# Optimization experiments

Measured on AMD Instinct MI355X. Metric: run time of the kernel, lower is better.

The kernel has to match this reference:

```python
import jax, jax.numpy as jnp
import numpy as np

N = 50000
E = 800000
NFEAT, NHID, NCLASS = 128, 128, 40


def setup_inputs() -> dict:
    key = jax.random.key(0)
    ks = jax.random.split(key, 8)
    x = jax.random.normal(ks[0], (N, NFEAT), dtype=jnp.float32)
    edge_index = jax.random.randint(ks[1], (2, E), 0, N, dtype=jnp.int64)
    def glorot(k, fan_in, fan_out):
        s = jnp.sqrt(6.0 / (fan_in + fan_out)).astype(jnp.float32)
        return jax.random.uniform(k, (fan_in, fan_out), jnp.float32, -s, s)
    W1 = glorot(ks[2], NFEAT, NHID); b1 = jnp.zeros((NHID,), jnp.float32)
    W2 = glorot(ks[3], NHID, NHID);  b2 = jnp.zeros((NHID,), jnp.float32)
    W3 = glorot(ks[4], NHID, NCLASS); b3 = jnp.zeros((NCLASS,), jnp.float32)
    return {"x": x, "edge_index": edge_index,
            "W1": W1, "b1": b1, "W2": W2, "b2": b2, "W3": W3, "b3": b3}


def _gcn_norm(edge_index, num_nodes, dtype):
    # Add self-loops, then symmetric normalization D^-1/2 (A+I) D^-1/2 (PyG gcn_norm).
    loop = jnp.arange(num_nodes, dtype=edge_index.dtype)
    src = jnp.concatenate([edge_index[0], loop])
    dst = jnp.concatenate([edge_index[1], loop])
    deg = jax.ops.segment_sum(jnp.ones_like(src, dtype=dtype), dst, num_segments=num_nodes)
    dinv = jnp.where(deg > 0, deg ** -0.5, 0.0).astype(dtype)
    norm = dinv[src] * dinv[dst]  # [E+N]
    return src, dst, norm


def _gcn_conv(h, src, dst, norm, W, b, num_nodes):
    h = h @ W                              # dense transform first (out_dim small)
    msg = h[src] * norm[:, None]           # gather + per-edge scale
    out = jax.ops.segment_sum(msg, dst, num_segments=num_nodes)  # scatter-add
    return out + b


def reference(x, edge_index, W1, b1, W2, b2, W3, b3):
    src, dst, norm = _gcn_norm(edge_index, N, x.dtype)
    h = jax.nn.relu(_gcn_conv(x, src, dst, norm, W1, b1, N))  # dropout: eval mode (identity)
    h = jax.nn.relu(_gcn_conv(h, src, dst, norm, W2, b2, N))
    h = _gcn_conv(h, src, dst, norm, W3, b3, N)
    return jax.nn.log_softmax(h, axis=-1)
```

## Files before the change

kernel.cpp:

```cpp
#include <hip/hip_runtime.h>
#include <stdint.h>

#define NN 50000
#define NE 800000
#define GG 782
#define NB 196
#define EB 3125

typedef __attribute__((ext_vector_type(8))) short bfx8;
typedef __attribute__((ext_vector_type(4))) float f32x4;

__device__ inline unsigned short f2bf(float f) {
    union { float f; uint32_t u; } x; x.f = f;
    uint32_t u = x.u;
    return (unsigned short)((u + 0x7fffu + ((u >> 16) & 1u)) >> 16);
}
__device__ inline uint32_t pack2bf(float lo, float hi) {
    return (uint32_t)f2bf(lo) | ((uint32_t)f2bf(hi) << 16);
}
__device__ inline float bf2f(unsigned short h) {
    union { uint32_t u; float f; } c; c.u = ((uint32_t)h) << 16;
    return c.f;
}
__device__ inline float2 bfp2f2(uint32_t v) {
    union { uint32_t u; float f; } a, b;
    a.u = (v & 0xffffu) << 16;
    b.u = v & 0xffff0000u;
    return make_float2(a.f, b.f);
}
__device__ inline bfx8 ld8(const unsigned short* p) {
    union { uint4 u; bfx8 v; } c;
    c.u = *(const uint4*)p;
    return c.v;
}
__device__ inline bfx8 cvt8(float4 u, float4 v) {
    union { unsigned short s[8]; bfx8 r; } c;
    c.s[0] = f2bf(u.x); c.s[1] = f2bf(u.y); c.s[2] = f2bf(u.z); c.s[3] = f2bf(u.w);
    c.s[4] = f2bf(v.x); c.s[5] = f2bf(v.y); c.s[6] = f2bf(v.z); c.s[7] = f2bf(v.w);
    return c.r;
}

__global__ void prep(const float* __restrict__ W1, const float* __restrict__ W2,
                     const float* __restrict__ W3,
                     unsigned short* __restrict__ WT1, unsigned short* __restrict__ WT2,
                     unsigned short* __restrict__ WT3, int* __restrict__ hist) {
    int bid = blockIdx.x;
    if (bid < 152) {
        int w = bid * 256 + threadIdx.x;
        if (w < 16384) {
            int nn = w >> 7, k = w & 127;
            WT1[nn * 128 + k] = f2bf(W1[k * 128 + nn]);
        } else if (w < 32768) {
            int w2 = w - 16384, nn = w2 >> 7, k = w2 & 127;
            WT2[nn * 128 + k] = f2bf(W2[k * 128 + nn]);
        } else if (w < 38912) {
            int w2 = w - 32768, nn = w2 >> 7, k = w2 & 127;
            WT3[nn * 128 + k] = (nn < 40) ? f2bf(W3[k * 40 + nn]) : (unsigned short)0;
        }
    } else {
        int i = (bid - 152) * 256 + threadIdx.x;
        if (i < NN) hist[i] = 0;
    }
}

__global__ __launch_bounds__(256) void gemm1_hist(const float* __restrict__ X,
                                                  const unsigned short* __restrict__ WT,
                                                  unsigned short* __restrict__ G, int n,
                                                  const int* __restrict__ dst,
                                                  int* __restrict__ hist,
                                                  unsigned short* __restrict__ rank, int e) {
    if (blockIdx.x >= GG) {
        int i = (blockIdx.x - GG) * 256 + threadIdx.x;
        if (i < e) rank[i] = (unsigned short)atomicAdd(hist + dst[i], 1);
        return;
    }
    int wave = threadIdx.x >> 6;
    int lane = threadIdx.x & 63;
    int quad = lane >> 4;
    int c = lane & 15;
    int rowbase = blockIdx.x * 64 + wave * 16;

    int arow = rowbase + c;
    if (arow >= n) arow = n - 1;
    const float* ap = X + (size_t)arow * 128 + quad * 8;
    bfx8 a[4];
#pragma unroll
    for (int kc = 0; kc < 4; kc++) {
        float4 u = *(const float4*)(ap + kc * 32);
        float4 v = *(const float4*)(ap + kc * 32 + 4);
        a[kc] = cvt8(u, v);
    }

    f32x4 acc[8];
#pragma unroll
    for (int ct = 0; ct < 8; ct++) acc[ct] = (f32x4){0.f, 0.f, 0.f, 0.f};
#pragma unroll
    for (int ct = 0; ct < 8; ct++) {
        const unsigned short* bp = WT + (size_t)(ct * 16 + c) * 128 + quad * 8;
#pragma unroll
        for (int kc = 0; kc < 4; kc++) {
            bfx8 b = ld8(bp + kc * 32);
            acc[ct] = __builtin_amdgcn_mfma_f32_16x16x32_bf16(a[kc], b, acc[ct], 0, 0, 0);
        }
    }

    int r0 = rowbase + quad * 4;
    bool odd = lane & 1;
#pragma unroll
    for (int ct = 0; ct < 8; ct++) {
        float x0 = acc[ct][0], x1 = acc[ct][1], x2 = acc[ct][2], x3 = acc[ct][3];
        float y0 = __shfl_xor(x0, 1, 64), y1 = __shfl_xor(x1, 1, 64);
        float y2 = __shfl_xor(x2, 1, 64), y3 = __shfl_xor(x3, 1, 64);
        int colp = ct * 16 + (c & ~1);
        if (!odd) {
            if (r0 + 0 < n) *(uint32_t*)(&G[(size_t)(r0 + 0) * 128 + colp]) = pack2bf(x0, y0);
            if (r0 + 1 < n) *(uint32_t*)(&G[(size_t)(r0 + 1) * 128 + colp]) = pack2bf(x1, y1);
        } else {
            if (r0 + 2 < n) *(uint32_t*)(&G[(size_t)(r0 + 2) * 128 + colp]) = pack2bf(y2, x2);
            if (r0 + 3 < n) *(uint32_t*)(&G[(size_t)(r0 + 3) * 128 + colp]) = pack2bf(y3, x3);
        }
    }
}

__global__ void scan_dinv(const int* __restrict__ hist, int* row_ptr, int* bsum,
                          float* dinv, int n) {
    __shared__ int s[256];
    int tid = threadIdx.x;
    int i = blockIdx.x * 256 + tid;
    int v = (i < n) ? hist[i] : 0;
    s[tid] = v;
    __syncthreads();
#pragma unroll
    for (int off = 1; off < 256; off <<= 1) {
        int y = (tid >= off) ? s[tid - off] : 0;
        __syncthreads();
        s[tid] += y;
        __syncthreads();
    }
    if (i < n) {
        row_ptr[i] = s[tid] - v;
        dinv[i] = rsqrtf(1.0f + (float)v);
    }
    if (tid == 255) bsum[blockIdx.x] = s[255];
}

__global__ void bucket_k(const int* __restrict__ src, const int* __restrict__ dst,
                         const int* __restrict__ row_ptr, const int* __restrict__ bsum,
                         const unsigned short* __restrict__ rank,
                         unsigned short* __restrict__ csr_src, int* __restrict__ boff_g,
                         int e) {
    __shared__ int s[256];
    __shared__ int bex[256];
    int tid = threadIdx.x;
    int v = (tid < NB) ? bsum[tid] : 0;
    s[tid] = v;
    __syncthreads();
#pragma unroll
    for (int off = 1; off < 256; off <<= 1) {
        int y = (tid >= off) ? s[tid - off] : 0;
        __syncthreads();
        s[tid] += y;
        __syncthreads();
    }
    bex[tid] = s[tid] - v;
    __syncthreads();

    if (blockIdx.x == gridDim.x - 1) {
        if (tid < NB) boff_g[tid] = bex[tid];
        return;
    }
    int i = blockIdx.x * 256 + tid;
    if (i < e) {
        int d = dst[i];
        csr_src[row_ptr[d] + bex[d >> 8] + (int)rank[i]] = (unsigned short)src[i];
    }
}

__global__ __launch_bounds__(256) void gemm128_mfma(const unsigned short* __restrict__ A,
                                                    const unsigned short* __restrict__ WT,
                                                    const float* __restrict__ dinv,
                                                    unsigned short* __restrict__ G, int n) {
    int wave = threadIdx.x >> 6;
    int lane = threadIdx.x & 63;
    int quad = lane >> 4;
    int c = lane & 15;
    int rowbase = blockIdx.x * 64 + wave * 16;

    int arow = rowbase + c;
    if (arow >= n) arow = n - 1;
    const unsigned short* ap = A + (size_t)arow * 128 + quad * 8;
    bfx8 a[4];
#pragma unroll
    for (int kc = 0; kc < 4; kc++) a[kc] = ld8(ap + kc * 32);

    f32x4 acc[8];
#pragma unroll
    for (int ct = 0; ct < 8; ct++) acc[ct] = (f32x4){0.f, 0.f, 0.f, 0.f};
#pragma unroll
    for (int ct = 0; ct < 8; ct++) {
        const unsigned short* bp = WT + (size_t)(ct * 16 + c) * 128 + quad * 8;
#pragma unroll
        for (int kc = 0; kc < 4; kc++) {
            bfx8 b = ld8(bp + kc * 32);
            acc[ct] = __builtin_amdgcn_mfma_f32_16x16x32_bf16(a[kc], b, acc[ct], 0, 0, 0);
        }
    }

    int r0 = rowbase + quad * 4;
    float di[4];
#pragma unroll
    for (int r = 0; r < 4; r++) {
        int rr = r0 + r;
        di[r] = dinv[rr < n ? rr : 0];
    }
    bool odd = lane & 1;
#pragma unroll
    for (int ct = 0; ct < 8; ct++) {
        float x0 = acc[ct][0], x1 = acc[ct][1], x2 = acc[ct][2], x3 = acc[ct][3];
        float y0 = __shfl_xor(x0, 1, 64), y1 = __shfl_xor(x1, 1, 64);
        float y2 = __shfl_xor(x2, 1, 64), y3 = __shfl_xor(x3, 1, 64);
        int colp = ct * 16 + (c & ~1);
        if (!odd) {
            if (r0 + 0 < n) *(uint32_t*)(&G[(size_t)(r0 + 0) * 128 + colp]) = pack2bf(di[0] * x0, di[0] * y0);
            if (r0 + 1 < n) *(uint32_t*)(&G[(size_t)(r0 + 1) * 128 + colp]) = pack2bf(di[1] * x1, di[1] * y1);
        } else {
            if (r0 + 2 < n) *(uint32_t*)(&G[(size_t)(r0 + 2) * 128 + colp]) = pack2bf(di[2] * y2, di[2] * x2);
            if (r0 + 3 < n) *(uint32_t*)(&G[(size_t)(r0 + 3) * 128 + colp]) = pack2bf(di[3] * y3, di[3] * x3);
        }
    }
}

__global__ __launch_bounds__(256) void gemm40_mfma(const unsigned short* __restrict__ A,
                                                   const unsigned short* __restrict__ WT,
                                                   const float* __restrict__ dinv,
                                                   unsigned short* __restrict__ G, int n) {
    int wave = threadIdx.x >> 6;
    int lane = threadIdx.x & 63;
    int quad = lane >> 4;
    int c = lane & 15;
    int rowbase = blockIdx.x * 64 + wave * 16;

    int arow = rowbase + c;
    if (arow >= n) arow = n - 1;
    const unsigned short* ap = A + (size_t)arow * 128 + quad * 8;
    bfx8 a[4];
#pragma unroll
    for (int kc = 0; kc < 4; kc++) a[kc] = ld8(ap + kc * 32);

    f32x4 acc[3];
#pragma unroll
    for (int ct = 0; ct < 3; ct++) acc[ct] = (f32x4){0.f, 0.f, 0.f, 0.f};
#pragma unroll
    for (int ct = 0; ct < 3; ct++) {
        const unsigned short* bp = WT + (size_t)(ct * 16 + c) * 128 + quad * 8;
#pragma unroll
        for (int kc = 0; kc < 4; kc++) {
            bfx8 b = ld8(bp + kc * 32);
            acc[ct] = __builtin_amdgcn_mfma_f32_16x16x32_bf16(a[kc], b, acc[ct], 0, 0, 0);
        }
    }

    int r0 = rowbase + quad * 4;
    float di[4];
#pragma unroll
    for (int r = 0; r < 4; r++) {
        int rr = r0 + r;
        di[r] = dinv[rr < n ? rr : 0];
    }
    bool odd = lane & 1;
#pragma unroll
    for (int ct = 0; ct < 3; ct++) {
        float x0 = acc[ct][0], x1 = acc[ct][1], x2 = acc[ct][2], x3 = acc[ct][3];
        float y0 = __shfl_xor(x0, 1, 64), y1 = __shfl_xor(x1, 1, 64);
        float y2 = __shfl_xor(x2, 1, 64), y3 = __shfl_xor(x3, 1, 64);
        int colp = ct * 16 + (c & ~1);
        if (colp >= 40) continue;
        if (!odd) {
            if (r0 + 0 < n) *(uint32_t*)(&G[(size_t)(r0 + 0) * 40 + colp]) = pack2bf(di[0] * x0, di[0] * y0);
            if (r0 + 1 < n) *(uint32_t*)(&G[(size_t)(r0 + 1) * 40 + colp]) = pack2bf(di[1] * x1, di[1] * y1);
        } else {
            if (r0 + 2 < n) *(uint32_t*)(&G[(size_t)(r0 + 2) * 40 + colp]) = pack2bf(di[2] * y2, di[2] * x2);
            if (r0 + 3 < n) *(uint32_t*)(&G[(size_t)(r0 + 3) * 40 + colp]) = pack2bf(di[3] * y3, di[3] * x3);
        }
    }
}

__global__ __launch_bounds__(256) void agg128_l1(const unsigned short* __restrict__ G,
                                                 const int* __restrict__ row_ptr,
                                                 const int* __restrict__ boff,
                                                 const int* __restrict__ hist,
                                                 const unsigned short* __restrict__ csr_src,
                                                 const float* __restrict__ dinv,
                                                 const float* __restrict__ b,
                                                 unsigned short* __restrict__ Y, int n) {
    int node = blockIdx.x * 4 + (threadIdx.x >> 6);
    if (node >= n) return;
    int l = threadIdx.x & 63;
    const uint32_t* Gr = (const uint32_t*)G;

    float dn = dinv[node];
    float2 sf = bfp2f2(Gr[(size_t)node * 64 + l]);
    float2 acc = make_float2(dn * sf.x, dn * sf.y);
    int p = row_ptr[node] + boff[node >> 8];
    int p1 = p + hist[node];
    for (; p + 7 < p1; p += 8) {
        int s0 = csr_src[p],     s1 = csr_src[p + 1], s2 = csr_src[p + 2], s3 = csr_src[p + 3];
        int s4 = csr_src[p + 4], s5 = csr_src[p + 5], s6 = csr_src[p + 6], s7 = csr_src[p + 7];
        float d0 = dinv[s0], d1 = dinv[s1], d2 = dinv[s2], d3 = dinv[s3];
        float d4 = dinv[s4], d5 = dinv[s5], d6 = dinv[s6], d7 = dinv[s7];
        float2 f0 = bfp2f2(Gr[(size_t)s0 * 64 + l]), f1 = bfp2f2(Gr[(size_t)s1 * 64 + l]);
        float2 f2 = bfp2f2(Gr[(size_t)s2 * 64 + l]), f3 = bfp2f2(Gr[(size_t)s3 * 64 + l]);
        float2 f4 = bfp2f2(Gr[(size_t)s4 * 64 + l]), f5 = bfp2f2(Gr[(size_t)s5 * 64 + l]);
        float2 f6 = bfp2f2(Gr[(size_t)s6 * 64 + l]), f7 = bfp2f2(Gr[(size_t)s7 * 64 + l]);
        acc.x += (fmaf(d0, f0.x, d1 * f1.x) + fmaf(d2, f2.x, d3 * f3.x)) +
                 (fmaf(d4, f4.x, d5 * f5.x) + fmaf(d6, f6.x, d7 * f7.x));
        acc.y += (fmaf(d0, f0.y, d1 * f1.y) + fmaf(d2, f2.y, d3 * f3.y)) +
                 (fmaf(d4, f4.y, d5 * f5.y) + fmaf(d6, f6.y, d7 * f7.y));
    }
    for (; p < p1; ++p) {
        int s = csr_src[p];
        float ds = dinv[s];
        float2 f = bfp2f2(Gr[(size_t)s * 64 + l]);
        acc.x = fmaf(ds, f.x, acc.x);
        acc.y = fmaf(ds, f.y, acc.y);
    }
    float vx = fmaf(dn, acc.x, b[2 * l]);
    float vy = fmaf(dn, acc.y, b[2 * l + 1]);
    ((uint32_t*)Y)[(size_t)node * 64 + l] = pack2bf(vx > 0.f ? vx : 0.f, vy > 0.f ? vy : 0.f);
}

__global__ __launch_bounds__(256) void agg128(const unsigned short* __restrict__ G,
                                              const int* __restrict__ row_ptr,
                                              const int* __restrict__ boff,
                                              const int* __restrict__ hist,
                                              const unsigned short* __restrict__ csr_src,
                                              const float* __restrict__ dinv,
                                              const float* __restrict__ b,
                                              unsigned short* __restrict__ Y, int n) {
    int node = blockIdx.x * 4 + (threadIdx.x >> 6);
    if (node >= n) return;
    int l = threadIdx.x & 63;
    const uint32_t* Gr = (const uint32_t*)G;

    float2 acc = bfp2f2(Gr[(size_t)node * 64 + l]);
    int p = row_ptr[node] + boff[node >> 8];
    int p1 = p + hist[node];
    for (; p + 7 < p1; p += 8) {
        int s0 = csr_src[p],     s1 = csr_src[p + 1], s2 = csr_src[p + 2], s3 = csr_src[p + 3];
        int s4 = csr_src[p + 4], s5 = csr_src[p + 5], s6 = csr_src[p + 6], s7 = csr_src[p + 7];
        float2 f0 = bfp2f2(Gr[(size_t)s0 * 64 + l]), f1 = bfp2f2(Gr[(size_t)s1 * 64 + l]);
        float2 f2 = bfp2f2(Gr[(size_t)s2 * 64 + l]), f3 = bfp2f2(Gr[(size_t)s3 * 64 + l]);
        float2 f4 = bfp2f2(Gr[(size_t)s4 * 64 + l]), f5 = bfp2f2(Gr[(size_t)s5 * 64 + l]);
        float2 f6 = bfp2f2(Gr[(size_t)s6 * 64 + l]), f7 = bfp2f2(Gr[(size_t)s7 * 64 + l]);
        acc.x += ((f0.x + f1.x) + (f2.x + f3.x)) + ((f4.x + f5.x) + (f6.x + f7.x));
        acc.y += ((f0.y + f1.y) + (f2.y + f3.y)) + ((f4.y + f5.y) + (f6.y + f7.y));
    }
    for (; p < p1; ++p) {
        float2 f = bfp2f2(Gr[(size_t)csr_src[p] * 64 + l]);
        acc.x += f.x; acc.y += f.y;
    }
    float dn = dinv[node];
    float vx = fmaf(dn, acc.x, b[2 * l]);
    float vy = fmaf(dn, acc.y, b[2 * l + 1]);
    ((uint32_t*)Y)[(size_t)node * 64 + l] = pack2bf(vx > 0.f ? vx : 0.f, vy > 0.f ? vy : 0.f);
}

__global__ __launch_bounds__(256) void agg40_lsm(const unsigned short* __restrict__ G,
                                                 const int* __restrict__ row_ptr,
                                                 const int* __restrict__ boff,
                                                 const int* __restrict__ hist,
                                                 const unsigned short* __restrict__ csr_src,
                                                 const float* __restrict__ dinv,
                                                 const float* __restrict__ b,
                                                 float* __restrict__ Y, int n) {
    int node = blockIdx.x * 4 + (threadIdx.x >> 6);
    if (node >= n) return;
    int lane = threadIdx.x & 63;
    bool act = lane < 40;
    int lc = act ? lane : 0;

    float acc = act ? bf2f(G[(size_t)node * 40 + lane]) : 0.f;
    int p = row_ptr[node] + boff[node >> 8];
    int p1 = p + hist[node];
    for (; p + 3 < p1; p += 4) {
        int s0 = csr_src[p], s1 = csr_src[p + 1], s2 = csr_src[p + 2], s3 = csr_src[p + 3];
        float f0 = bf2f(G[(size_t)s0 * 40 + lc]);
        float f1 = bf2f(G[(size_t)s1 * 40 + lc]);
        float f2 = bf2f(G[(size_t)s2 * 40 + lc]);
        float f3 = bf2f(G[(size_t)s3 * 40 + lc]);
        acc += (f0 + f1) + (f2 + f3);
    }
    for (; p < p1; ++p) acc += bf2f(G[(size_t)csr_src[p] * 40 + lc]);

    float v = act ? fmaf(dinv[node], acc, b[lane]) : -1e30f;
    float m = v;
#pragma unroll
    for (int off = 32; off > 0; off >>= 1) m = fmaxf(m, __shfl_xor(m, off, 64));
    float ex = act ? expf(v - m) : 0.f;
    float s_ = ex;
#pragma unroll
    for (int off = 32; off > 0; off >>= 1) s_ += __shfl_xor(s_, off, 64);
    float ls = logf(s_);
    if (act) Y[(size_t)node * 40 + lane] = v - m - ls;
}


extern "C" void kernel_launch(void* const* d_in, const int* in_sizes, int n_in,
                              void* d_out, int out_size, void* d_ws, size_t ws_size,
                              hipStream_t stream) {
    const float* x  = (const float*)d_in[0];
    const int*   ei = (const int*)d_in[1];
    const float* W1 = (const float*)d_in[2];
    const float* b1 = (const float*)d_in[3];
    const float* W2 = (const float*)d_in[4];
    const float* b2 = (const float*)d_in[5];
    const float* W3 = (const float*)d_in[6];
    const float* b3 = (const float*)d_in[7];
    float* out = (float*)d_out;

    const int n = NN, e = NE;
    const int* srcI = ei;
    const int* dstI = ei + e;

    char* ws = (char*)d_ws;
    int*            hist    = (int*)ws;
    int*            row_ptr = (int*)(ws + 200704);
    int*            bsum    = (int*)(ws + 401408);
    int*            boff    = (int*)(ws + 402432);
    float*          dinv    = (float*)(ws + 403456);
    unsigned short* rank    = (unsigned short*)(ws + 604160);
    unsigned short* csr_src = (unsigned short*)(ws + 2204160);
    unsigned short* WT1     = (unsigned short*)(ws + 3804160);
    unsigned short* WT2     = (unsigned short*)(ws + 3836928);
    unsigned short* WT3     = (unsigned short*)(ws + 3869696);
    unsigned short* bufG    = (unsigned short*)(ws + 3881984);
    unsigned short* bufA    = (unsigned short*)(ws + 16681984);

    prep<<<152 + NB, 256, 0, stream>>>(W1, W2, W3, WT1, WT2, WT3, hist);
    gemm1_hist<<<GG + EB, 256, 0, stream>>>(x, WT1, bufG, n, dstI, hist, rank, e);
    scan_dinv<<<NB, 256, 0, stream>>>(hist, row_ptr, bsum, dinv, n);
    bucket_k<<<EB + 1, 256, 0, stream>>>(srcI, dstI, row_ptr, bsum, rank, csr_src, boff, e);
    agg128_l1<<<(n + 3) / 4, 256, 0, stream>>>(bufG, row_ptr, boff, hist, csr_src, dinv, b1, bufA, n);
    gemm128_mfma<<<GG, 256, 0, stream>>>(bufA, WT2, dinv, bufG, n);
    agg128<<<(n + 3) / 4, 256, 0, stream>>>(bufG, row_ptr, boff, hist, csr_src, dinv, b2, bufA, n);
    gemm40_mfma<<<GG, 256, 0, stream>>>(bufA, WT3, dinv, bufG, n);
    agg40_lsm<<<(n + 3) / 4, 256, 0, stream>>>(bufG, row_ptr, boff, hist, csr_src, dinv, b3, out, n);
}
```

Baseline: 296.9 us.

## Replicate degree histogram across 16 copies to reduce atomic contention

The in-degree histogram is split into 16 replicas, with each edge block atomically incrementing the replica chosen by its block index. The scan kernel merges the replicas into per-node degrees and per-replica offsets, and the bucket kernel adds the replica offset when placing edges into CSR. The aim is to spread atomic traffic on the same destination counters. In exchange it zeroes and reads 16 times as much histogram memory, and it stores the histogram and offsets in the bufA region that is reused later.

```diff
diff --git a/kernel.cpp b/kernel.cpp
--- a/kernel.cpp
+++ b/kernel.cpp
@@ -6,6 +6,8 @@
 #define GG 782
 #define NB 196
 #define EB 3125
+#define RR 16
+#define RZB 3125
 
 typedef __attribute__((ext_vector_type(8))) short bfx8;
 typedef __attribute__((ext_vector_type(4))) float f32x4;
@@ -59,7 +61,7 @@
         }
     } else {
         int i = (bid - 152) * 256 + threadIdx.x;
-        if (i < NN) hist[i] = 0;
+        if (i < RR * NN) hist[i] = 0;
     }
 }
 
@@ -70,8 +72,12 @@
                                                   int* __restrict__ hist,
                                                   unsigned short* __restrict__ rank, int e) {
     if (blockIdx.x >= GG) {
-        int i = (blockIdx.x - GG) * 256 + threadIdx.x;
-        if (i < e) rank[i] = (unsigned short)atomicAdd(hist + dst[i], 1);
+        int be = blockIdx.x - GG;
+        int i = be * 256 + threadIdx.x;
+        if (i < e) {
+            int r = be & (RR - 1);
+            rank[i] = (unsigned short)atomicAdd(hist + r * NN + dst[i], 1);
+        }
         return;
     }
     int wave = threadIdx.x >> 6;
@@ -123,11 +129,23 @@
 }
 
 __global__ void scan_dinv(const int* __restrict__ hist, int* row_ptr, int* bsum,
-                          float* dinv, int n) {
+                          float* dinv, int* __restrict__ deg,
+                          unsigned short* __restrict__ repoff, int n) {
     __shared__ int s[256];
     int tid = threadIdx.x;
     int i = blockIdx.x * 256 + tid;
-    int v = (i < n) ? hist[i] : 0;
+    int v = 0;
+    if (i < n) {
+        int off = 0;
+#pragma unroll
+        for (int r = 0; r < RR; r++) {
+            int h = hist[r * NN + i];
+            repoff[r * NN + i] = (unsigned short)off;
+            off += h;
+        }
+        v = off;
+        deg[i] = v;
+    }
     s[tid] = v;
     __syncthreads();
 #pragma unroll
@@ -147,6 +165,7 @@
 __global__ void bucket_k(const int* __restrict__ src, const int* __restrict__ dst,
                          const int* __restrict__ row_ptr, const int* __restrict__ bsum,
                          const unsigned short* __restrict__ rank,
+                         const unsigned short* __restrict__ repoff,
                          unsigned short* __restrict__ csr_src, int* __restrict__ boff_g,
                          int e) {
     __shared__ int s[256];
@@ -172,7 +191,9 @@
     int i = blockIdx.x * 256 + tid;
     if (i < e) {
         int d = dst[i];
-        csr_src[row_ptr[d] + bex[d >> 8] + (int)rank[i]] = (unsigned short)src[i];
+        int r = blockIdx.x & (RR - 1);
+        csr_src[row_ptr[d] + bex[d >> 8] + (int)repoff[r * NN + d] + (int)rank[i]] =
+            (unsigned short)src[i];
     }
 }
 
@@ -423,7 +444,7 @@
     const int* dstI = ei + e;
 
     char* ws = (char*)d_ws;
-    int*            hist    = (int*)ws;
+    int*            deg     = (int*)ws;
     int*            row_ptr = (int*)(ws + 200704);
     int*            bsum    = (int*)(ws + 401408);
     int*            boff    = (int*)(ws + 402432);
@@ -435,14 +456,16 @@
     unsigned short* WT3     = (unsigned short*)(ws + 3869696);
     unsigned short* bufG    = (unsigned short*)(ws + 3881984);
     unsigned short* bufA    = (unsigned short*)(ws + 16681984);
-
-    prep<<<152 + NB, 256, 0, stream>>>(W1, W2, W3, WT1, WT2, WT3, hist);
-    gemm1_hist<<<GG + EB, 256, 0, stream>>>(x, WT1, bufG, n, dstI, hist, rank, e);
-    scan_dinv<<<NB, 256, 0, stream>>>(hist, row_ptr, bsum, dinv, n);
-    bucket_k<<<EB + 1, 256, 0, stream>>>(srcI, dstI, row_ptr, bsum, rank, csr_src, boff, e);
-    agg128_l1<<<(n + 3) / 4, 256, 0, stream>>>(bufG, row_ptr, boff, hist, csr_src, dinv, b1, bufA, n);
+    int*            hist16  = (int*)(ws + 16681984);
+    unsigned short* repoff  = (unsigned short*)(ws + 16681984 + RR * NN * 4);
+
+    prep<<<152 + RZB, 256, 0, stream>>>(W1, W2, W3, WT1, WT2, WT3, hist16);
+    gemm1_hist<<<GG + EB, 256, 0, stream>>>(x, WT1, bufG, n, dstI, hist16, rank, e);
+    scan_dinv<<<NB, 256, 0, stream>>>(hist16, row_ptr, bsum, dinv, deg, repoff, n);
+    bucket_k<<<EB + 1, 256, 0, stream>>>(srcI, dstI, row_ptr, bsum, rank, repoff, csr_src, boff, e);
+    agg128_l1<<<(n + 3) / 4, 256, 0, stream>>>(bufG, row_ptr, boff, deg, csr_src, dinv, b1, bufA, n);
     gemm128_mfma<<<GG, 256, 0, stream>>>(bufA, WT2, dinv, bufG, n);
-    agg128<<<(n + 3) / 4, 256, 0, stream>>>(bufG, row_ptr, boff, hist, csr_src, dinv, b2, bufA, n);
+    agg128<<<(n + 3) / 4, 256, 0, stream>>>(bufG, row_ptr, boff, deg, csr_src, dinv, b2, bufA, n);
     gemm40_mfma<<<GG, 256, 0, stream>>>(bufA, WT3, dinv, bufG, n);
-    agg40_lsm<<<(n + 3) / 4, 256, 0, stream>>>(bufG, row_ptr, boff, hist, csr_src, dinv, b3, out, n);
-}
+    agg40_lsm<<<(n + 3) / 4, 256, 0, stream>>>(bufG, row_ptr, boff, deg, csr_src, dinv, b3, out, n);
+}
```

Result: no change. 294.8 us (-0.7%).

## Replace global-atomic CSR build with two-pass LDS bucket sort

Applied to the files above, without the earlier changes.

Replaces the per-edge global atomic histogram and rank-based scatter with a two-level bucket sort. Edges are first counted per high-byte bucket in LDS and scattered into packed (dst,src) words by tile, then each bucket block sorts by low byte in LDS to emit row_ptr, degree, dinv and csr_src. This removes 800k contended global atomics and the rank array, at the cost of an extra pass over the packed edges and a single-block scan kernel. Within-node edge order becomes nondeterministic, which changes float summation order.

```diff
diff --git a/kernel.cpp b/kernel.cpp
--- a/kernel.cpp
+++ b/kernel.cpp
@@ -5,7 +5,8 @@
 #define NE 800000
 #define GG 782
 #define NB 196
-#define EB 3125
+#define TT 8192
+#define TB 98
 
 typedef __attribute__((ext_vector_type(8))) short bfx8;
 typedef __attribute__((ext_vector_type(4))) float f32x4;
@@ -43,23 +44,17 @@
 __global__ void prep(const float* __restrict__ W1, const float* __restrict__ W2,
                      const float* __restrict__ W3,
                      unsigned short* __restrict__ WT1, unsigned short* __restrict__ WT2,
-                     unsigned short* __restrict__ WT3, int* __restrict__ hist) {
-    int bid = blockIdx.x;
-    if (bid < 152) {
-        int w = bid * 256 + threadIdx.x;
-        if (w < 16384) {
-            int nn = w >> 7, k = w & 127;
-            WT1[nn * 128 + k] = f2bf(W1[k * 128 + nn]);
-        } else if (w < 32768) {
-            int w2 = w - 16384, nn = w2 >> 7, k = w2 & 127;
-            WT2[nn * 128 + k] = f2bf(W2[k * 128 + nn]);
-        } else if (w < 38912) {
-            int w2 = w - 32768, nn = w2 >> 7, k = w2 & 127;
-            WT3[nn * 128 + k] = (nn < 40) ? f2bf(W3[k * 40 + nn]) : (unsigned short)0;
-        }
-    } else {
-        int i = (bid - 152) * 256 + threadIdx.x;
-        if (i < NN) hist[i] = 0;
+                     unsigned short* __restrict__ WT3) {
+    int w = blockIdx.x * 256 + threadIdx.x;
+    if (w < 16384) {
+        int nn = w >> 7, k = w & 127;
+        WT1[nn * 128 + k] = f2bf(W1[k * 128 + nn]);
+    } else if (w < 32768) {
+        int w2 = w - 16384, nn = w2 >> 7, k = w2 & 127;
+        WT2[nn * 128 + k] = f2bf(W2[k * 128 + nn]);
+    } else if (w < 38912) {
+        int w2 = w - 32768, nn = w2 >> 7, k = w2 & 127;
+        WT3[nn * 128 + k] = (nn < 40) ? f2bf(W3[k * 40 + nn]) : (unsigned short)0;
     }
 }
 
@@ -67,11 +62,19 @@
                                                   const unsigned short* __restrict__ WT,
                                                   unsigned short* __restrict__ G, int n,
                                                   const int* __restrict__ dst,
-                                                  int* __restrict__ hist,
-                                                  unsigned short* __restrict__ rank, int e) {
+                                                  int* __restrict__ counts, int e) {
     if (blockIdx.x >= GG) {
-        int i = (blockIdx.x - GG) * 256 + threadIdx.x;
-        if (i < e) rank[i] = (unsigned short)atomicAdd(hist + dst[i], 1);
+        int b = blockIdx.x - GG;
+        __shared__ int h[256];
+        h[threadIdx.x] = 0;
+        __syncthreads();
+        int start = b * TT;
+        int end = start + TT; if (end > e) end = e;
+        for (int i = start + threadIdx.x; i < end; i += 256)
+            atomicAdd(&h[dst[i] >> 8], 1);
+        __syncthreads();
+        int d = threadIdx.x;
+        if (d < NB) counts[d * TB + b] = h[d];
         return;
     }
     int wave = threadIdx.x >> 6;
@@ -122,57 +125,103 @@
     }
 }
 
-__global__ void scan_dinv(const int* __restrict__ hist, int* row_ptr, int* bsum,
-                          float* dinv, int n) {
+__global__ void scanA(int* __restrict__ counts, int* __restrict__ base196) {
     __shared__ int s[256];
-    int tid = threadIdx.x;
-    int i = blockIdx.x * 256 + tid;
-    int v = (i < n) ? hist[i] : 0;
-    s[tid] = v;
+    int d = threadIdx.x;
+    int run = 0;
+    if (d < NB) {
+        for (int b0 = 0; b0 < TB; b0 += 14) {
+            int c[14];
+#pragma unroll
+            for (int j = 0; j < 14; j++) {
+                int b = b0 + j;
+                c[j] = (b < TB) ? counts[d * TB + b] : 0;
+            }
+#pragma unroll
+            for (int j = 0; j < 14; j++) {
+                int b = b0 + j;
+                if (b < TB) counts[d * TB + b] = run;
+                run += c[j];
+            }
+        }
+    }
+    int v = run;
+    s[d] = v;
     __syncthreads();
 #pragma unroll
     for (int off = 1; off < 256; off <<= 1) {
-        int y = (tid >= off) ? s[tid - off] : 0;
-        __syncthreads();
-        s[tid] += y;
-        __syncthreads();
-    }
-    if (i < n) {
-        row_ptr[i] = s[tid] - v;
-        dinv[i] = rsqrtf(1.0f + (float)v);
-    }
-    if (tid == 255) bsum[blockIdx.x] = s[255];
-}
-
-__global__ void bucket_k(const int* __restrict__ src, const int* __restrict__ dst,
-                         const int* __restrict__ row_ptr, const int* __restrict__ bsum,
-                         const unsigned short* __restrict__ rank,
-                         unsigned short* __restrict__ csr_src, int* __restrict__ boff_g,
-                         int e) {
+        int y = (d >= off) ? s[d - off] : 0;
+        __syncthreads();
+        s[d] += y;
+        __syncthreads();
+    }
+    if (d <= NB) base196[d] = s[d] - v;
+}
+
+__global__ __launch_bounds__(256) void scatterA(const int* __restrict__ src,
+                                                const int* __restrict__ dst,
+                                                const int* __restrict__ counts,
+                                                const int* __restrict__ base196,
+                                                uint32_t* __restrict__ packA, int e) {
+    __shared__ int gb[256];
+    __shared__ int lc[256];
+    int t = threadIdx.x;
+    if (t < NB) {
+        gb[t] = base196[t] + counts[t * TB + blockIdx.x];
+        lc[t] = 0;
+    }
+    __syncthreads();
+    int start = blockIdx.x * TT;
+    int end = start + TT; if (end > e) end = e;
+    for (int i = start + t; i < end; i += 256) {
+        int d = dst[i];
+        int s = src[i];
+        int hi = d >> 8;
+        int r = atomicAdd(&lc[hi], 1);
+        packA[gb[hi] + r] = ((uint32_t)d << 16) | (uint32_t)s;
+    }
+}
+
+__global__ __launch_bounds__(256) void buildB(const uint32_t* __restrict__ packA,
+                                              const int* __restrict__ base196,
+                                              int* __restrict__ row_ptr, int* __restrict__ deg,
+                                              float* __restrict__ dinv,
+                                              unsigned short* __restrict__ csr_src, int n) {
+    __shared__ int cnt[256];
     __shared__ int s[256];
-    __shared__ int bex[256];
-    int tid = threadIdx.x;
-    int v = (tid < NB) ? bsum[tid] : 0;
-    s[tid] = v;
+    __shared__ int rp[256];
+    int hi = blockIdx.x;
+    int t = threadIdx.x;
+    cnt[t] = 0;
+    __syncthreads();
+    int b0 = base196[hi], b1 = base196[hi + 1];
+    for (int i = b0 + t; i < b1; i += 256)
+        atomicAdd(&cnt[(packA[i] >> 16) & 0xFF], 1);
+    __syncthreads();
+    int v = cnt[t];
+    s[t] = v;
     __syncthreads();
 #pragma unroll
     for (int off = 1; off < 256; off <<= 1) {
-        int y = (tid >= off) ? s[tid - off] : 0;
-        __syncthreads();
-        s[tid] += y;
-        __syncthreads();
-    }
-    bex[tid] = s[tid] - v;
-    __syncthreads();
-
-    if (blockIdx.x == gridDim.x - 1) {
-        if (tid < NB) boff_g[tid] = bex[tid];
-        return;
-    }
-    int i = blockIdx.x * 256 + tid;
-    if (i < e) {
-        int d = dst[i];
-        csr_src[row_ptr[d] + bex[d >> 8] + (int)rank[i]] = (unsigned short)src[i];
+        int y = (t >= off) ? s[t - off] : 0;
+        __syncthreads();
+        s[t] += y;
+        __syncthreads();
+    }
+    rp[t] = b0 + s[t] - v;
+    int node = hi * 256 + t;
+    if (node < n) {
+        row_ptr[node] = rp[t];
+        deg[node] = v;
+        dinv[node] = rsqrtf(1.0f + (float)v);
+    }
+    cnt[t] = 0;
+    __syncthreads();
+    for (int i = b0 + t; i < b1; i += 256) {
+        uint32_t p = packA[i];
+        int lo = (p >> 16) & 0xFF;
+        int r = atomicAdd(&cnt[lo], 1);
+        csr_src[rp[lo] + r] = (unsigned short)(p & 0xFFFF);
     }
 }
 
@@ -287,8 +336,7 @@
 
 __global__ __launch_bounds__(256) void agg128_l1(const unsigned short* __restrict__ G,
                                                  const int* __restrict__ row_ptr,
-                                                 const int* __restrict__ boff,
-                                                 const int* __restrict__ hist,
+                                                 const int* __restrict__ deg,
                                                  const unsigned short* __restrict__ csr_src,
                                                  const float* __restrict__ dinv,
                                                  const float* __restrict__ b,
@@ -301,8 +349,8 @@
     float dn = dinv[node];
     float2 sf = bfp2f2(Gr[(size_t)node * 64 + l]);
     float2 acc = make_float2(dn * sf.x, dn * sf.y);
-    int p = row_ptr[node] + boff[node >> 8];
-    int p1 = p + hist[node];
+    int p = row_ptr[node];
+    int p1 = p + deg[node];
     for (; p + 7 < p1; p += 8) {
         int s0 = csr_src[p],     s1 = csr_src[p + 1], s2 = csr_src[p + 2], s3 = csr_src[p + 3];
         int s4 = csr_src[p + 4], s5 = csr_src[p + 5], s6 = csr_src[p + 6], s7 = csr_src[p + 7];
@@ -331,8 +379,7 @@
 
 __global__ __launch_bounds__(256) void agg128(const unsigned short* __restrict__ G,
                                               const int* __restrict__ row_ptr,
-                                              const int* __restrict__ boff,
-                                              const int* __restrict__ hist,
+                                              const int* __restrict__ deg,
                                               const unsigned short* __restrict__ csr_src,
                                               const float* __restrict__ dinv,
                                               const float* __restrict__ b,
@@ -343,8 +390,8 @@
     const uint32_t* Gr = (const uint32_t*)G;
 
     float2 acc = bfp2f2(Gr[(size_t)node * 64 + l]);
-    int p = row_ptr[node] + boff[node >> 8];
-    int p1 = p + hist[node];
+    int p = row_ptr[node];
+    int p1 = p + deg[node];
     for (; p + 7 < p1; p += 8) {
         int s0 = csr_src[p],     s1 = csr_src[p + 1], s2 = csr_src[p + 2], s3 = csr_src[p + 3];
         int s4 = csr_src[p + 4], s5 = csr_src[p + 5], s6 = csr_src[p + 6], s7 = csr_src[p + 7];
@@ -367,8 +414,7 @@
 
 __global__ __launch_bounds__(256) void agg40_lsm(const unsigned short* __restrict__ G,
                                                  const int* __restrict__ row_ptr,
-                                                 const int* __restrict__ boff,
-                                                 const int* __restrict__ hist,
+                                                 const int* __restrict__ deg,
                                                  const unsigned short* __restrict__ csr_src,
                                                  const float* __restrict__ dinv,
                                                  const float* __restrict__ b,
@@ -380,8 +426,8 @@
     int lc = act ? lane : 0;
 
     float acc = act ? bf2f(G[(size_t)node * 40 + lane]) : 0.f;
-    int p = row_ptr[node] + boff[node >> 8];
-    int p1 = p + hist[node];
+    int p = row_ptr[node];
+    int p1 = p + deg[node];
     for (; p + 3 < p1; p += 4) {
         int s0 = csr_src[p], s1 = csr_src[p + 1], s2 = csr_src[p + 2], s3 = csr_src[p + 3];
         float f0 = bf2f(G[(size_t)s0 * 40 + lc]);
@@ -423,26 +469,27 @@
     const int* dstI = ei + e;
 
     char* ws = (char*)d_ws;
-    int*            hist    = (int*)ws;
+    int*            deg     = (int*)ws;
     int*            row_ptr = (int*)(ws + 200704);
-    int*            bsum    = (int*)(ws + 401408);
-    int*            boff    = (int*)(ws + 402432);
-    float*          dinv    = (float*)(ws + 403456);
-    unsigned short* rank    = (unsigned short*)(ws + 604160);
-    unsigned short* csr_src = (unsigned short*)(ws + 2204160);
-    unsigned short* WT1     = (unsigned short*)(ws + 3804160);
-    unsigned short* WT2     = (unsigned short*)(ws + 3836928);
-    unsigned short* WT3     = (unsigned short*)(ws + 3869696);
-    unsigned short* bufG    = (unsigned short*)(ws + 3881984);
-    unsigned short* bufA    = (unsigned short*)(ws + 16681984);
-
-    prep<<<152 + NB, 256, 0, stream>>>(W1, W2, W3, WT1, WT2, WT3, hist);
-    gemm1_hist<<<GG + EB, 256, 0, stream>>>(x, WT1, bufG, n, dstI, hist, rank, e);
-    scan_dinv<<<NB, 256, 0, stream>>>(hist, row_ptr, bsum, dinv, n);
-    bucket_k<<<EB + 1, 256, 0, stream>>>(srcI, dstI, row_ptr, bsum, rank, csr_src, boff, e);
-    agg128_l1<<<(n + 3) / 4, 256, 0, stream>>>(bufG, row_ptr, boff, hist, csr_src, dinv, b1, bufA, n);
+    float*          dinv    = (float*)(ws + 401408);
+    int*            base196 = (int*)(ws + 602112);
+    int*            counts  = (int*)(ws + 603136);
+    uint32_t*       packA   = (uint32_t*)(ws + 681984);
+    unsigned short* csr_src = (unsigned short*)(ws + 3881984);
+    unsigned short* WT1     = (unsigned short*)(ws + 5481984);
+    unsigned short* WT2     = (unsigned short*)(ws + 5514752);
+    unsigned short* WT3     = (unsigned short*)(ws + 5547520);
+    unsigned short* bufG    = (unsigned short*)(ws + 5559808);
+    unsigned short* bufA    = (unsigned short*)(ws + 18359808);
+
+    prep<<<152, 256, 0, stream>>>(W1, W2, W3, WT1, WT2, WT3);
+    gemm1_hist<<<GG + TB, 256, 0, stream>>>(x, WT1, bufG, n, dstI, counts, e);
+    scanA<<<1, 256, 0, stream>>>(counts, base196);
+    scatterA<<<TB, 256, 0, stream>>>(srcI, dstI, counts, base196, packA, e);
+    buildB<<<NB, 256, 0, stream>>>(packA, base196, row_ptr, deg, dinv, csr_src, n);
+    agg128_l1<<<(n + 3) / 4, 256, 0, stream>>>(bufG, row_ptr, deg, csr_src, dinv, b1, bufA, n);
     gemm128_mfma<<<GG, 256, 0, stream>>>(bufA, WT2, dinv, bufG, n);
-    agg128<<<(n + 3) / 4, 256, 0, stream>>>(bufG, row_ptr, boff, hist, csr_src, dinv, b2, bufA, n);
+    agg128<<<(n + 3) / 4, 256, 0, stream>>>(bufG, row_ptr, deg, csr_src, dinv, b2, bufA, n);
     gemm40_mfma<<<GG, 256, 0, stream>>>(bufA, WT3, dinv, bufG, n);
-    agg40_lsm<<<(n + 3) / 4, 256, 0, stream>>>(bufG, row_ptr, boff, hist, csr_src, dinv, b3, out, n);
-}
+    agg40_lsm<<<(n + 3) / 4, 256, 0, stream>>>(bufG, row_ptr, deg, csr_src, dinv, b3, out, n);
+}
```

Result: faster. 290.7 us (-2.1%).
